# Performance work log

Hardware: AMD Instinct MI355X
Metric: run time of the kernel (lower is better)

## Reference

```python
import jax, jax.numpy as jnp
import numpy as np

B, S, H = 4, 512, 256

def setup_inputs() -> dict:
    key = jax.random.key(0)
    k1, k2, k3, k4 = jax.random.split(key, 4)
    scale = 1.0 / np.sqrt(H)
    return {
        "h": jax.random.normal(k1, (B, S, H), dtype=jnp.float32),
        "W_t": jax.random.normal(k2, (H, H), dtype=jnp.float32) * scale,
        "W_t_prime": jax.random.normal(k3, (H, H), dtype=jnp.float32) * scale,
        "b_h": jnp.zeros((H,), dtype=jnp.float32),
        "W_a": jax.random.normal(k4, (H,), dtype=jnp.float32) * scale,
        "b_a": jnp.zeros((), dtype=jnp.float32),
    }

def reference(h, W_t, W_t_prime, b_h, W_a, b_a):
    # Project once per timestep, then broadcast-add over the (t, t') pair grid.
    ht = jnp.einsum("bsh,hk->bsk", h, W_t)          # W_t applied to h^t
    htp = jnp.einsum("bsh,hk->bsk", h, W_t_prime)   # W_{t'} applied to h^{t'}
    # transformed: (B, S_t, S_t', H)
    transformed = ht[:, :, None, :] + htp[:, None, :, :] + b_h
    tanh_out = jnp.tanh(transformed)
    scores = jnp.einsum("bsth,h->bst", tanh_out, W_a) + b_a  # (B, S, S)
    scores = jax.nn.sigmoid(scores)
    attention_weights = jax.nn.softmax(scores, axis=2)
    output = jnp.einsum("bst,bth->bsh", attention_weights, h)
    return output, attention_weights
```

## Files before the change

kernel.cpp:

```cpp
#include <hip/hip_runtime.h>

#define Bn 4
#define Sn 512
#define Hn 256

#define CC   2.8853900817779268f
#define L2E  1.4426950408889634f

typedef __attribute__((ext_vector_type(4))) float f32x4;
typedef __attribute__((ext_vector_type(8))) short short8;

__device__ __forceinline__ unsigned short bf16rn(float f) {
    unsigned int u = __float_as_uint(f);
    u += 0x7fffu + ((u >> 16) & 1u);
    return (unsigned short)(u >> 16);
}
__device__ __forceinline__ float bf16tof(unsigned short b) {
    return __uint_as_float(((unsigned int)b) << 16);
}

__global__ __launch_bounds__(512) void gemm_kernel(
    const float* __restrict__ h,  const float* __restrict__ Wt,
    const float* __restrict__ Wp, const float* __restrict__ Wa,
    const float* __restrict__ ba, const float* __restrict__ bh,
    float* __restrict__ Egt, float* __restrict__ Egp4,
    float* __restrict__ wa2, float* __restrict__ cst)
{
    __shared__ char lds[152640];
    unsigned short* A1 = (unsigned short*)lds;
    unsigned short* A2 = (unsigned short*)(lds + 33792);
    unsigned short* B1 = (unsigned short*)(lds + 67584);
    unsigned short* B2 = (unsigned short*)(lds + 101376);
    float* tile = (float*)(lds + 135168);
    float* red4 = (float*)(lds + 152576);

    const int tid = threadIdx.x;
    const int mb  = blockIdx.x >> 3;
    const int nb  = blockIdx.x & 7;
    const int m0  = mb * 64;
    const bool isT = (nb < 4);
    const int n0  = (isT ? nb : nb - 4) * 64;
    const float* __restrict__ W = isT ? Wt : Wp;

    if (blockIdx.x == 0) {
        if (tid < 256) {
            float wv = Wa[tid];
#pragma unroll
            for (int off = 32; off >= 1; off >>= 1) wv += __shfl_xor(wv, off, 64);
            if ((tid & 63) == 0) red4[tid >> 6] = wv;
        }
        __syncthreads();
        if (tid < 256) wa2[tid] = -2.0f * Wa[tid];
        if (tid == 0)
            cst[0] = -L2E * ((red4[0] + red4[1] + red4[2] + red4[3]) + ba[0]);
    }

    {
        const int row = tid >> 3;
        const int seg = (tid & 7) * 32;
        const float* __restrict__ src = h + (m0 + row) * Hn + seg;
        unsigned int* d1 = (unsigned int*)A1 + (row * 264 + seg) / 2;
        unsigned int* d2 = (unsigned int*)A2 + (row * 264 + seg) / 2;
#pragma unroll
        for (int i = 0; i < 8; i++) {
            const float4 v = ((const float4*)src)[i];
            const float f[4] = {v.x, v.y, v.z, v.w};
            unsigned short b1[4], b2[4];
#pragma unroll
            for (int j = 0; j < 4; j++) {
                b1[j] = bf16rn(f[j]);
                b2[j] = bf16rn(f[j] - bf16tof(b1[j]));
            }
            d1[2 * i]     = (unsigned)b1[0] | ((unsigned)b1[1] << 16);
            d1[2 * i + 1] = (unsigned)b1[2] | ((unsigned)b1[3] << 16);
            d2[2 * i]     = (unsigned)b2[0] | ((unsigned)b2[1] << 16);
            d2[2 * i + 1] = (unsigned)b2[2] | ((unsigned)b2[3] << 16);
        }
    }

    for (int kt = 0; kt < 4; kt++) {
        const int k0 = kt * 64;
        __syncthreads();
#pragma unroll
        for (int i = 0; i < 2; i++) {
            const int idx = tid + 512 * i;
            const int kr = idx >> 4, nq = idx & 15;
            *(float4*)&tile[kr * 68 + nq * 4] =
                *(const float4*)&W[(k0 + kr) * Hn + n0 + nq * 4];
        }
        __syncthreads();
#pragma unroll
        for (int i = 0; i < 4; i++) {
            const int idx = tid + 512 * i;
            const int n = idx >> 5, kp = idx & 31;
            const float f0 = tile[(2 * kp) * 68 + n];
            const float f1 = tile[(2 * kp + 1) * 68 + n];
            const unsigned short a0 = bf16rn(f0), a1 = bf16rn(f1);
            const unsigned short c0 = bf16rn(f0 - bf16tof(a0));
            const unsigned short c1 = bf16rn(f1 - bf16tof(a1));
            ((unsigned int*)B1)[n * 132 + k0 / 2 + kp] =
                (unsigned)a0 | ((unsigned)a1 << 16);
            ((unsigned int*)B2)[n * 132 + k0 / 2 + kp] =
                (unsigned)c0 | ((unsigned)c1 << 16);
        }
    }
    __syncthreads();

    const int w    = tid >> 6;
    const int w2   = w & 3;
    const int mh   = w >> 2;
    const int lane = tid & 63;
    const int quad = lane >> 4;
    const int l15  = lane & 15;

    f32x4 acc[2];
#pragma unroll
    for (int i = 0; i < 2; i++) acc[i] = (f32x4){0.f, 0.f, 0.f, 0.f};

#pragma unroll 2
    for (int ks = 0; ks < 256; ks += 32) {
        const int bof = (w2 * 16 + l15) * 264 + ks + quad * 8;
        const short8 b1 = *(const short8*)(B1 + bof);
        const short8 b2 = *(const short8*)(B2 + bof);
#pragma unroll
        for (int mi = 0; mi < 2; mi++) {
            const int mt = mh * 2 + mi;
            const int aof = (mt * 16 + l15) * 264 + ks + quad * 8;
            const short8 a1 = *(const short8*)(A1 + aof);
            const short8 a2 = *(const short8*)(A2 + aof);
            acc[mi] = __builtin_amdgcn_mfma_f32_16x16x32_bf16(a1, b1, acc[mi], 0, 0, 0);
            acc[mi] = __builtin_amdgcn_mfma_f32_16x16x32_bf16(a1, b2, acc[mi], 0, 0, 0);
            acc[mi] = __builtin_amdgcn_mfma_f32_16x16x32_bf16(a2, b1, acc[mi], 0, 0, 0);
        }
    }

    __syncthreads();
    float* ct = tile;
#pragma unroll
    for (int mi = 0; mi < 2; mi++) {
        const int mt = mh * 2 + mi;
#pragma unroll
        for (int r = 0; r < 4; r++)
            ct[(mt * 16 + quad * 4 + r) * 68 + w2 * 16 + l15] = acc[mi][r];
    }
    __syncthreads();

    const int b  = m0 >> 9;
    const int s0 = m0 & 511;
    if (isT) {
        const int n0g = nb * 64;
#pragma unroll
        for (int i = 0; i < 2; i++) {
            const int item = tid + i * 512;
            const int mr = item >> 4, nq = item & 15;
            const float4 c  = *(const float4*)&ct[mr * 68 + nq * 4];
            const float4 bv = *(const float4*)&bh[n0g + nq * 4];
            float4 o;
            o.x = __builtin_amdgcn_exp2f((c.x + bv.x) * CC);
            o.y = __builtin_amdgcn_exp2f((c.y + bv.y) * CC);
            o.z = __builtin_amdgcn_exp2f((c.z + bv.z) * CC);
            o.w = __builtin_amdgcn_exp2f((c.w + bv.w) * CC);
            *(float4*)&Egt[(m0 + mr) * Hn + n0g + nq * 4] = o;
        }
    } else {
        const int kq0 = (nb - 4) * 16;
#pragma unroll
        for (int i = 0; i < 2; i++) {
            const int item = tid + i * 512;
            const int mr = item & 63, nq = item >> 6;
            const float4 c = *(const float4*)&ct[mr * 68 + nq * 4];
            float4 o;
            o.x = __builtin_amdgcn_exp2f(c.x * CC);
            o.y = __builtin_amdgcn_exp2f(c.y * CC);
            o.z = __builtin_amdgcn_exp2f(c.z * CC);
            o.w = __builtin_amdgcn_exp2f(c.w * CC);
            *(float4*)&Egp4[b * 131072 + (kq0 + nq) * 2048 + (s0 + mr) * 4] = o;
        }
    }
}

__global__ __launch_bounds__(1024) void attn_kernel(
    const float* __restrict__ hsrc, const float* __restrict__ Egt,
    const float* __restrict__ Egp4, const float* __restrict__ wa2,
    const float* __restrict__ cst,
    float* __restrict__ out, float* __restrict__ out_attn)
{
    __shared__ char smem[40960];
    float*  attn_l = (float*)smem;
    float*  accl   = (float*)(smem + 8192);
    float*  red    = (float*)(smem + 16384);
    float4* part   = (float4*)(smem + 8192);

    const int tid = threadIdx.x;
    const int tp  = tid & 511;
    const int kh  = tid >> 9;
    const int b   = blockIdx.x & 3;
    const int t0  = (blockIdx.x >> 2) << 2;

    const int kbu = __builtin_amdgcn_readfirstlane(kh << 5);

    const float* __restrict__ egt = Egt + (b * Sn + t0) * Hn;
    const float4* __restrict__ ep = (const float4*)(Egp4 + b * (Hn * Sn));

    float acc[4] = {0.f, 0.f, 0.f, 0.f};

    float4 w4c  = *(const float4*)&wa2[kbu * 4];
    float4 eg0c = *(const float4*)&egt[0 * Hn + kbu * 4];
    float4 eg1c = *(const float4*)&egt[1 * Hn + kbu * 4];
    float4 eg2c = *(const float4*)&egt[2 * Hn + kbu * 4];
    float4 eg3c = *(const float4*)&egt[3 * Hn + kbu * 4];

#pragma unroll 2
    for (int kk = 0; kk < 32; kk++) {
        const int k4n = kbu + ((kk + 1) & 31);
        const float4 w4n  = *(const float4*)&wa2[k4n * 4];
        const float4 eg0n = *(const float4*)&egt[0 * Hn + k4n * 4];
        const float4 eg1n = *(const float4*)&egt[1 * Hn + k4n * 4];
        const float4 eg2n = *(const float4*)&egt[2 * Hn + k4n * 4];
        const float4 eg3n = *(const float4*)&egt[3 * Hn + k4n * 4];

        const float4 cur = ep[(kbu + kk) * Sn + tp];

        const float4 egs[4] = {eg0c, eg1c, eg2c, eg3c};
#pragma unroll
        for (int r = 0; r < 4; r++) {
            const float4 eg = egs[r];
            const float d1 = fmaf(cur.x, eg.x, 1.0f);
            const float d2 = fmaf(cur.y, eg.y, 1.0f);
            const float d3 = fmaf(cur.z, eg.z, 1.0f);
            const float d4 = fmaf(cur.w, eg.w, 1.0f);
            const float p12 = d1 * d2, p34 = d3 * d4;
            const float n12 = fmaf(w4c.x, d2, w4c.y * d1);
            const float n34 = fmaf(w4c.z, d4, w4c.w * d3);
            const float num = fmaf(n12, p34, n34 * p12);
            acc[r] = fmaf(num, __builtin_amdgcn_rcpf(p12 * p34), acc[r]);
        }

        w4c = w4n; eg0c = eg0n; eg1c = eg1n; eg2c = eg2n; eg3c = eg3n;
    }

    if (kh == 1) {
#pragma unroll
        for (int r = 0; r < 4; r++) accl[r * 512 + tp] = acc[r];
    }
    __syncthreads();

    float ex[4];
    const float k0 = cst[0];
    if (kh == 0) {
#pragma unroll
        for (int r = 0; r < 4; r++) {
            const float a   = acc[r] + accl[r * 512 + tp];
            const float e1  = __builtin_amdgcn_exp2f(fmaf(-L2E, a, k0));
            const float sig = __builtin_amdgcn_rcpf(1.0f + e1);
            ex[r] = __builtin_amdgcn_exp2f(L2E * sig);
        }
        const int lane = tid & 63, wid = tid >> 6;
#pragma unroll
        for (int r = 0; r < 4; r++) {
            float v = ex[r];
#pragma unroll
            for (int off = 32; off >= 1; off >>= 1) v += __shfl_xor(v, off, 64);
            if (lane == 0) red[r * 8 + wid] = v;
        }
    }
    __syncthreads();

    if (kh == 0) {
#pragma unroll
        for (int r = 0; r < 4; r++) {
            float tot = 0.f;
#pragma unroll
            for (int i = 0; i < 8; i++) tot += red[r * 8 + i];
            const float a = ex[r] * __builtin_amdgcn_rcpf(tot);
            attn_l[r * Sn + tp] = a;
            out_attn[(b * Sn + t0 + r) * Sn + tp] = a;
        }
    }
    __syncthreads();

    const int c4 = tid & 63;
    const int q  = tid >> 6;

    const float* __restrict__ hb = hsrc + (b * Sn + q * 32) * Hn + c4 * 4;

    float4 a4[4];
#pragma unroll
    for (int r = 0; r < 4; r++) a4[r] = (float4){0.f, 0.f, 0.f, 0.f};

#pragma unroll 2
    for (int j4 = 0; j4 < 8; j4++) {
        float4 wv[4];
#pragma unroll
        for (int r = 0; r < 4; r++)
            wv[r] = *(const float4*)&attn_l[r * Sn + q * 32 + j4 * 4];
#pragma unroll
        for (int i = 0; i < 4; i++) {
            const float4 hv = *(const float4*)&hb[(j4 * 4 + i) * Hn];
#pragma unroll
            for (int r = 0; r < 4; r++) {
                const float wr = ((const float*)&wv[r])[i];
                a4[r].x = fmaf(wr, hv.x, a4[r].x);
                a4[r].y = fmaf(wr, hv.y, a4[r].y);
                a4[r].z = fmaf(wr, hv.z, a4[r].z);
                a4[r].w = fmaf(wr, hv.w, a4[r].w);
            }
        }
    }
    __syncthreads();

    if (q < 8) {
#pragma unroll
        for (int r = 0; r < 4; r++) part[(q * 4 + r) * 64 + c4] = a4[r];
    }
    __syncthreads();
    if (q >= 8) {
#pragma unroll
        for (int r = 0; r < 4; r++) {
            float4 p = part[((q - 8) * 4 + r) * 64 + c4];
            p.x += a4[r].x; p.y += a4[r].y; p.z += a4[r].z; p.w += a4[r].w;
            part[((q - 8) * 4 + r) * 64 + c4] = p;
        }
    }
    __syncthreads();

    {
        const int col = tid & 255;
        const int r   = tid >> 8;
        const float* pf = (const float*)part;
        float s = 0.f;
#pragma unroll
        for (int qq = 0; qq < 8; qq++)
            s += pf[((qq * 4 + r) * 64 + (col >> 2)) * 4 + (col & 3)];
        out[(b * Sn + t0 + r) * Hn + col] = s;
    }
}

extern "C" void kernel_launch(void* const* d_in, const int* in_sizes, int n_in,
                              void* d_out, int out_size, void* d_ws, size_t ws_size,
                              hipStream_t stream) {
    const float* h   = (const float*)d_in[0];
    const float* Wt  = (const float*)d_in[1];
    const float* Wtp = (const float*)d_in[2];
    const float* bh  = (const float*)d_in[3];
    const float* Wa  = (const float*)d_in[4];
    const float* ba  = (const float*)d_in[5];

    float* out      = (float*)d_out;
    float* out_attn = out + Bn * Sn * Hn;

    float* ws   = (float*)d_ws;
    float* Egt  = ws;
    float* Egp4 = ws + 524288;
    float* wa2  = ws + 1048576;
    float* cst  = ws + 1048832;

    gemm_kernel<<<dim3(256), dim3(512), 0, stream>>>(
        h, Wt, Wtp, Wa, ba, bh, Egt, Egp4, wa2, cst);
    attn_kernel<<<dim3(Bn * (Sn / 4)), dim3(1024), 0, stream>>>(
        h, Egt, Egp4, wa2, cst, out, out_attn);
}
```

Measured before the change: 112.7 us.

## Halve GEMM M-tile and split K staging to shrink LDS and double grid

The projection GEMM kernel now uses 32-row M tiles instead of 64 and stages the K dimension in two 128-wide halves, so the bf16 hi/lo operand buffers fit in about 60 KB of LDS instead of about 150 KB. The grid doubles to 512 blocks and launch bounds request more resident blocks per CU, aiming to raise occupancy and spread the small GEMM across more CUs. In exchange, each block redoes the W conversion for its tile, so W is loaded and split into bf16 pairs twice as often, and there are extra barriers between the K halves.

```diff
diff --git a/kernel.cpp b/kernel.cpp
--- a/kernel.cpp
+++ b/kernel.cpp
@@ -19,25 +19,25 @@
     return __uint_as_float(((unsigned int)b) << 16);
 }
 
-__global__ __launch_bounds__(512) void gemm_kernel(
+__global__ __launch_bounds__(512, 4) void gemm_kernel(
     const float* __restrict__ h,  const float* __restrict__ Wt,
     const float* __restrict__ Wp, const float* __restrict__ Wa,
     const float* __restrict__ ba, const float* __restrict__ bh,
     float* __restrict__ Egt, float* __restrict__ Egp4,
     float* __restrict__ wa2, float* __restrict__ cst)
 {
-    __shared__ char lds[152640];
+    __shared__ char lds[60944];
     unsigned short* A1 = (unsigned short*)lds;
-    unsigned short* A2 = (unsigned short*)(lds + 33792);
-    unsigned short* B1 = (unsigned short*)(lds + 67584);
-    unsigned short* B2 = (unsigned short*)(lds + 101376);
-    float* tile = (float*)(lds + 135168);
-    float* red4 = (float*)(lds + 152576);
+    unsigned short* A2 = (unsigned short*)(lds + 8704);
+    unsigned short* B1 = (unsigned short*)(lds + 17408);
+    unsigned short* B2 = (unsigned short*)(lds + 34816);
+    float* tile = (float*)(lds + 52224);
+    float* red4 = (float*)(lds + 60928);
 
     const int tid = threadIdx.x;
     const int mb  = blockIdx.x >> 3;
     const int nb  = blockIdx.x & 7;
-    const int m0  = mb * 64;
+    const int m0  = mb * 32;
     const bool isT = (nb < 4);
     const int n0  = (isT ? nb : nb - 4) * 64;
     const float* __restrict__ W = isT ? Wt : Wp;
@@ -54,57 +54,6 @@
         if (tid == 0)
             cst[0] = -L2E * ((red4[0] + red4[1] + red4[2] + red4[3]) + ba[0]);
     }
-
-    {
-        const int row = tid >> 3;
-        const int seg = (tid & 7) * 32;
-        const float* __restrict__ src = h + (m0 + row) * Hn + seg;
-        unsigned int* d1 = (unsigned int*)A1 + (row * 264 + seg) / 2;
-        unsigned int* d2 = (unsigned int*)A2 + (row * 264 + seg) / 2;
-#pragma unroll
-        for (int i = 0; i < 8; i++) {
-            const float4 v = ((const float4*)src)[i];
-            const float f[4] = {v.x, v.y, v.z, v.w};
-            unsigned short b1[4], b2[4];
-#pragma unroll
-            for (int j = 0; j < 4; j++) {
-                b1[j] = bf16rn(f[j]);
-                b2[j] = bf16rn(f[j] - bf16tof(b1[j]));
-            }
-            d1[2 * i]     = (unsigned)b1[0] | ((unsigned)b1[1] << 16);
-            d1[2 * i + 1] = (unsigned)b1[2] | ((unsigned)b1[3] << 16);
-            d2[2 * i]     = (unsigned)b2[0] | ((unsigned)b2[1] << 16);
-            d2[2 * i + 1] = (unsigned)b2[2] | ((unsigned)b2[3] << 16);
-        }
-    }
-
-    for (int kt = 0; kt < 4; kt++) {
-        const int k0 = kt * 64;
-        __syncthreads();
-#pragma unroll
-        for (int i = 0; i < 2; i++) {
-            const int idx = tid + 512 * i;
-            const int kr = idx >> 4, nq = idx & 15;
-            *(float4*)&tile[kr * 68 + nq * 4] =
-                *(const float4*)&W[(k0 + kr) * Hn + n0 + nq * 4];
-        }
-        __syncthreads();
-#pragma unroll
-        for (int i = 0; i < 4; i++) {
-            const int idx = tid + 512 * i;
-            const int n = idx >> 5, kp = idx & 31;
-            const float f0 = tile[(2 * kp) * 68 + n];
-            const float f1 = tile[(2 * kp + 1) * 68 + n];
-            const unsigned short a0 = bf16rn(f0), a1 = bf16rn(f1);
-            const unsigned short c0 = bf16rn(f0 - bf16tof(a0));
-            const unsigned short c1 = bf16rn(f1 - bf16tof(a1));
-            ((unsigned int*)B1)[n * 132 + k0 / 2 + kp] =
-                (unsigned)a0 | ((unsigned)a1 << 16);
-            ((unsigned int*)B2)[n * 132 + k0 / 2 + kp] =
-                (unsigned)c0 | ((unsigned)c1 << 16);
-        }
-    }
-    __syncthreads();
 
     const int w    = tid >> 6;
     const int w2   = w & 3;
@@ -113,69 +62,111 @@
     const int quad = lane >> 4;
     const int l15  = lane & 15;
 
-    f32x4 acc[2];
-#pragma unroll
-    for (int i = 0; i < 2; i++) acc[i] = (f32x4){0.f, 0.f, 0.f, 0.f};
-
-#pragma unroll 2
-    for (int ks = 0; ks < 256; ks += 32) {
-        const int bof = (w2 * 16 + l15) * 264 + ks + quad * 8;
-        const short8 b1 = *(const short8*)(B1 + bof);
-        const short8 b2 = *(const short8*)(B2 + bof);
-#pragma unroll
-        for (int mi = 0; mi < 2; mi++) {
-            const int mt = mh * 2 + mi;
-            const int aof = (mt * 16 + l15) * 264 + ks + quad * 8;
+    f32x4 acc = (f32x4){0.f, 0.f, 0.f, 0.f};
+
+    for (int kh2 = 0; kh2 < 2; kh2++) {
+        const int K0 = kh2 << 7;
+        __syncthreads();
+
+        {
+            const int row = tid >> 4;
+            const int seg = (tid & 15) * 8;
+            const float* __restrict__ src = h + (m0 + row) * Hn + K0 + seg;
+            unsigned int* d1 = (unsigned int*)A1 + row * 68 + (seg >> 1);
+            unsigned int* d2 = (unsigned int*)A2 + row * 68 + (seg >> 1);
+#pragma unroll
+            for (int i = 0; i < 2; i++) {
+                const float4 v = ((const float4*)src)[i];
+                const float f[4] = {v.x, v.y, v.z, v.w};
+                unsigned short b1[4], b2[4];
+#pragma unroll
+                for (int j = 0; j < 4; j++) {
+                    b1[j] = bf16rn(f[j]);
+                    b2[j] = bf16rn(f[j] - bf16tof(b1[j]));
+                }
+                d1[2 * i]     = (unsigned)b1[0] | ((unsigned)b1[1] << 16);
+                d1[2 * i + 1] = (unsigned)b1[2] | ((unsigned)b1[3] << 16);
+                d2[2 * i]     = (unsigned)b2[0] | ((unsigned)b2[1] << 16);
+                d2[2 * i + 1] = (unsigned)b2[2] | ((unsigned)b2[3] << 16);
+            }
+        }
+
+        for (int kt = 0; kt < 4; kt++) {
+            const int koff = K0 + kt * 32;
+            if (kt) __syncthreads();
+            {
+                const int kr = tid >> 4;
+                const int nq = tid & 15;
+                *(float4*)&tile[kr * 68 + nq * 4] =
+                    *(const float4*)&W[(koff + kr) * Hn + n0 + nq * 4];
+            }
+            __syncthreads();
+            {
+                const int n  = tid >> 3;
+                const int p0 = (tid & 7) * 2;
+                const float f0 = tile[(2 * p0    ) * 68 + n];
+                const float f1 = tile[(2 * p0 + 1) * 68 + n];
+                const float f2 = tile[(2 * p0 + 2) * 68 + n];
+                const float f3 = tile[(2 * p0 + 3) * 68 + n];
+                const unsigned short a0 = bf16rn(f0), a1 = bf16rn(f1);
+                const unsigned short a2 = bf16rn(f2), a3 = bf16rn(f3);
+                const unsigned short c0 = bf16rn(f0 - bf16tof(a0));
+                const unsigned short c1 = bf16rn(f1 - bf16tof(a1));
+                const unsigned short c2 = bf16rn(f2 - bf16tof(a2));
+                const unsigned short c3 = bf16rn(f3 - bf16tof(a3));
+                unsigned int* o1 = (unsigned int*)B1 + n * 68 + kt * 16 + p0;
+                unsigned int* o2 = (unsigned int*)B2 + n * 68 + kt * 16 + p0;
+                o1[0] = (unsigned)a0 | ((unsigned)a1 << 16);
+                o1[1] = (unsigned)a2 | ((unsigned)a3 << 16);
+                o2[0] = (unsigned)c0 | ((unsigned)c1 << 16);
+                o2[1] = (unsigned)c2 | ((unsigned)c3 << 16);
+            }
+        }
+        __syncthreads();
+
+#pragma unroll
+        for (int ks = 0; ks < 128; ks += 32) {
+            const int bof = (w2 * 16 + l15) * 136 + ks + quad * 8;
+            const short8 b1 = *(const short8*)(B1 + bof);
+            const short8 b2 = *(const short8*)(B2 + bof);
+            const int aof = (mh * 16 + l15) * 136 + ks + quad * 8;
             const short8 a1 = *(const short8*)(A1 + aof);
             const short8 a2 = *(const short8*)(A2 + aof);
-            acc[mi] = __builtin_amdgcn_mfma_f32_16x16x32_bf16(a1, b1, acc[mi], 0, 0, 0);
-            acc[mi] = __builtin_amdgcn_mfma_f32_16x16x32_bf16(a1, b2, acc[mi], 0, 0, 0);
-            acc[mi] = __builtin_amdgcn_mfma_f32_16x16x32_bf16(a2, b1, acc[mi], 0, 0, 0);
-        }
-    }
-
-    __syncthreads();
+            acc = __builtin_amdgcn_mfma_f32_16x16x32_bf16(a1, b1, acc, 0, 0, 0);
+            acc = __builtin_amdgcn_mfma_f32_16x16x32_bf16(a1, b2, acc, 0, 0, 0);
+            acc = __builtin_amdgcn_mfma_f32_16x16x32_bf16(a2, b1, acc, 0, 0, 0);
+        }
+    }
+
     float* ct = tile;
 #pragma unroll
-    for (int mi = 0; mi < 2; mi++) {
-        const int mt = mh * 2 + mi;
-#pragma unroll
-        for (int r = 0; r < 4; r++)
-            ct[(mt * 16 + quad * 4 + r) * 68 + w2 * 16 + l15] = acc[mi][r];
-    }
+    for (int r = 0; r < 4; r++)
+        ct[(mh * 16 + quad * 4 + r) * 68 + w2 * 16 + l15] = acc[r];
     __syncthreads();
 
     const int b  = m0 >> 9;
     const int s0 = m0 & 511;
     if (isT) {
         const int n0g = nb * 64;
-#pragma unroll
-        for (int i = 0; i < 2; i++) {
-            const int item = tid + i * 512;
-            const int mr = item >> 4, nq = item & 15;
-            const float4 c  = *(const float4*)&ct[mr * 68 + nq * 4];
-            const float4 bv = *(const float4*)&bh[n0g + nq * 4];
-            float4 o;
-            o.x = __builtin_amdgcn_exp2f((c.x + bv.x) * CC);
-            o.y = __builtin_amdgcn_exp2f((c.y + bv.y) * CC);
-            o.z = __builtin_amdgcn_exp2f((c.z + bv.z) * CC);
-            o.w = __builtin_amdgcn_exp2f((c.w + bv.w) * CC);
-            *(float4*)&Egt[(m0 + mr) * Hn + n0g + nq * 4] = o;
-        }
+        const int mr = tid >> 4, nq = tid & 15;
+        const float4 c  = *(const float4*)&ct[mr * 68 + nq * 4];
+        const float4 bv = *(const float4*)&bh[n0g + nq * 4];
+        float4 o;
+        o.x = __builtin_amdgcn_exp2f((c.x + bv.x) * CC);
+        o.y = __builtin_amdgcn_exp2f((c.y + bv.y) * CC);
+        o.z = __builtin_amdgcn_exp2f((c.z + bv.z) * CC);
+        o.w = __builtin_amdgcn_exp2f((c.w + bv.w) * CC);
+        *(float4*)&Egt[(m0 + mr) * Hn + n0g + nq * 4] = o;
     } else {
         const int kq0 = (nb - 4) * 16;
-#pragma unroll
-        for (int i = 0; i < 2; i++) {
-            const int item = tid + i * 512;
-            const int mr = item & 63, nq = item >> 6;
-            const float4 c = *(const float4*)&ct[mr * 68 + nq * 4];
-            float4 o;
-            o.x = __builtin_amdgcn_exp2f(c.x * CC);
-            o.y = __builtin_amdgcn_exp2f(c.y * CC);
-            o.z = __builtin_amdgcn_exp2f(c.z * CC);
-            o.w = __builtin_amdgcn_exp2f(c.w * CC);
-            *(float4*)&Egp4[b * 131072 + (kq0 + nq) * 2048 + (s0 + mr) * 4] = o;
-        }
+        const int mr = tid & 31, nq = tid >> 5;
+        const float4 c = *(const float4*)&ct[mr * 68 + nq * 4];
+        float4 o;
+        o.x = __builtin_amdgcn_exp2f(c.x * CC);
+        o.y = __builtin_amdgcn_exp2f(c.y * CC);
+        o.z = __builtin_amdgcn_exp2f(c.z * CC);
+        o.w = __builtin_amdgcn_exp2f(c.w * CC);
+        *(float4*)&Egp4[b * 131072 + (kq0 + nq) * 2048 + (s0 + mr) * 4] = o;
     }
 }
 
@@ -355,7 +346,7 @@
     float* wa2  = ws + 1048576;
     float* cst  = ws + 1048832;
 
-    gemm_kernel<<<dim3(256), dim3(512), 0, stream>>>(
+    gemm_kernel<<<dim3(512), dim3(512), 0, stream>>>(
         h, Wt, Wtp, Wa, ba, bh, Egt, Egp4, wa2, cst);
     attn_kernel<<<dim3(Bn * (Sn / 4)), dim3(1024), 0, stream>>>(
         h, Egt, Egp4, wa2, cst, out, out_attn);
```

New measurement: 113.0 us. No clear change (+0.3%).
